# Optimization experiments

Measured on AMD Instinct MI355X. Metric: run time of the kernel, lower is better.

The kernel has to match this reference:

```python
import jax, jax.numpy as jnp
import numpy as np

FG_THRESH = 0.5
BG_HI = 0.5
BG_LO = 0.0
CLS_LAMBDA = 1.0
BBOX2D_LAMBDA = 1.0
BBOX3D_LAMBDA = 1.0

A, FH, FW, STRIDE = 36, 32, 106, 16  # 36*32*106 = 122112 anchors
B, G, NC = 4, 64, 4


def _smooth_l1(x):
    ax = jnp.abs(x)
    return jnp.where(ax < 1.0, 0.5 * ax * ax, ax - 0.5)


def setup_inputs() -> dict:
    rng = np.random.RandomState(0)
    # anchors: [x1,y1,x2,y2, z, w3d, h3d, l3d, ry], centered at origin
    ws = rng.uniform(16, 256, A).astype(np.float32)
    hs = rng.uniform(16, 256, A).astype(np.float32)
    anchors = np.zeros((A, 9), np.float32)
    anchors[:, 0] = -ws / 2; anchors[:, 1] = -hs / 2
    anchors[:, 2] = ws / 2;  anchors[:, 3] = hs / 2
    anchors[:, 4] = rng.uniform(5, 50, A)
    anchors[:, 5:8] = rng.uniform(1, 5, (A, 3))
    anchors[:, 8] = rng.uniform(-np.pi, np.pi, A)
    # rois = anchors tiled over the feature grid (locate_anchors), col 4 = anchor idx
    sx, sy = np.meshgrid(np.arange(FW) * STRIDE, np.arange(FH) * STRIDE)
    shifts = np.stack([sx.ravel(), sy.ravel(), sx.ravel(), sy.ravel()], 1).astype(np.float32)
    N = FH * FW * A
    rois = np.zeros((N, 5), np.float32)
    rois[:, :4] = (shifts[:, None, :] + anchors[None, :, :4]).reshape(-1, 4)
    rois[:, 4] = np.tile(np.arange(A), FH * FW)
    # GT 2D boxes (x1,y1,x2,y2) inside the 1696x512 image
    gcx = rng.uniform(0, FW * STRIDE, (B, G)); gcy = rng.uniform(0, FH * STRIDE, (B, G))
    gw = rng.uniform(30, 200, (B, G)); gh = rng.uniform(30, 200, (B, G))
    gt_boxes = np.stack([gcx - gw / 2, gcy - gh / 2, gcx + gw / 2, gcy + gh / 2], -1).astype(np.float32)
    # GT 3D: projected 3D center (u,v), z, w3d, h3d, l3d, ry
    gt_boxes_3d = np.stack([
        gcx, gcy,
        rng.uniform(5, 50, (B, G)),
        rng.uniform(1, 5, (B, G)), rng.uniform(1, 5, (B, G)), rng.uniform(1, 5, (B, G)),
        rng.uniform(-np.pi, np.pi, (B, G)),
    ], -1).astype(np.float32)
    gt_labels = rng.randint(1, NC, (B, G)).astype(np.int32)
    bbox_means = (rng.randn(1, 11) * 0.01).astype(np.float32)
    bbox_stds = (0.1 + rng.rand(1, 11) * 0.2).astype(np.float32)
    key = jax.random.key(0)
    k1, k2, k3, k4 = jax.random.split(key, 4)
    return {
        "cls": jax.random.normal(k1, (B, N, NC), jnp.float32),
        "prob": jax.random.uniform(k2, (B, N, NC), jnp.float32),
        "bbox_2d": 0.1 * jax.random.normal(k3, (B, N, 4), jnp.float32),
        "bbox_3d": 0.1 * jax.random.normal(k4, (B, N, 7), jnp.float32),
        "rois": jnp.asarray(rois),
        "anchors": jnp.asarray(anchors),
        "bbox_means": jnp.asarray(bbox_means),
        "bbox_stds": jnp.asarray(bbox_stds),
        "gt_boxes": jnp.asarray(gt_boxes),
        "gt_boxes_3d": jnp.asarray(gt_boxes_3d),
        "gt_labels": jnp.asarray(gt_labels),
    }


def _loss(cls, prob, bbox_2d, bbox_3d, rois, anchors, bbox_means, bbox_stds,
          gt_boxes, gt_boxes_3d, gt_labels):
    # anchor geometry (the +1.0 convention matches the torch code)
    widths = rois[:, 2] - rois[:, 0] + 1.0          # [N]
    heights = rois[:, 3] - rois[:, 1] + 1.0
    ctr_x = rois[:, 0] + 0.5 * widths
    ctr_y = rois[:, 1] + 0.5 * heights
    aidx = rois[:, 4].astype(jnp.int32)
    src = anchors[aidx]                             # [N,9] gathered anchors

    # IoU between every roi and every GT: [B,N,G]
    rx1 = rois[None, :, None, 0]; ry1 = rois[None, :, None, 1]
    rx2 = rois[None, :, None, 2]; ry2 = rois[None, :, None, 3]
    gx1 = gt_boxes[:, None, :, 0]; gy1 = gt_boxes[:, None, :, 1]
    gx2 = gt_boxes[:, None, :, 2]; gy2 = gt_boxes[:, None, :, 3]
    iw = jnp.clip(jnp.minimum(rx2, gx2) - jnp.maximum(rx1, gx1) + 1.0, 0.0)
    ih = jnp.clip(jnp.minimum(ry2, gy2) - jnp.maximum(ry1, gy1) + 1.0, 0.0)
    inter = iw * ih
    area_r = (rx2 - rx1 + 1.0) * (ry2 - ry1 + 1.0)
    area_g = (gx2 - gx1 + 1.0) * (gy2 - gy1 + 1.0)
    ols = inter / (area_r + area_g - inter)         # [B,N,G]

    best_iou = jnp.max(ols, axis=-1)                # [B,N]
    best_gt = jnp.argmax(ols, axis=-1)              # [B,N]

    fg = best_iou >= FG_THRESH
    bg = (best_iou < BG_HI) & (best_iou >= BG_LO) & (~fg)

    matched_lbl = jnp.take_along_axis(gt_labels, best_gt, axis=1)   # [B,N]
    labels = jnp.where(fg, matched_lbl, 0)

    gb = jnp.take_along_axis(gt_boxes, best_gt[..., None], axis=1)  # [B,N,4]
    gw = gb[..., 2] - gb[..., 0] + 1.0
    gh = gb[..., 3] - gb[..., 1] + 1.0
    gcx = gb[..., 0] + 0.5 * gw
    gcy = gb[..., 1] + 0.5 * gh
    t2d = jnp.stack([
        (gcx - ctr_x) / widths,
        (gcy - ctr_y) / heights,
        jnp.log(gw / widths),
        jnp.log(gh / heights),
    ], -1)
    t2d = (t2d - bbox_means[0, 0:4]) / bbox_stds[0, 0:4]

    g3 = jnp.take_along_axis(gt_boxes_3d, best_gt[..., None], axis=1)  # [B,N,7]
    t3d = jnp.stack([
        (g3[..., 0] - ctr_x) / widths,
        (g3[..., 1] - ctr_y) / heights,
        g3[..., 2] - src[:, 4],
        jnp.log(g3[..., 3] / src[:, 5]),
        jnp.log(g3[..., 4] / src[:, 6]),
        jnp.log(g3[..., 5] / src[:, 7]),
        g3[..., 6] - src[:, 8],
    ], -1)
    t3d = (t3d - bbox_means[0, 4:11]) / bbox_stds[0, 4:11]

    # ---- losses
    w_fg = fg.astype(cls.dtype)
    n_fg = jnp.maximum(jnp.sum(w_fg), 1.0)
    loss_b2d = jnp.sum(jnp.sum(_smooth_l1(bbox_2d - t2d), -1) * w_fg) / n_fg
    loss_b3d = jnp.sum(jnp.sum(_smooth_l1(bbox_3d - t3d), -1) * w_fg) / n_fg

    w_cls = (fg | bg).astype(cls.dtype)
    logp = jax.nn.log_softmax(cls, axis=-1)
    ce = -jnp.take_along_axis(logp, labels[..., None], axis=-1)[..., 0]
    loss_cls = jnp.sum(ce * w_cls) / jnp.maximum(jnp.sum(w_cls), 1.0)

    return CLS_LAMBDA * loss_cls + BBOX2D_LAMBDA * loss_b2d + BBOX3D_LAMBDA * loss_b3d


def reference(cls, prob, bbox_2d, bbox_3d, rois, anchors, bbox_means, bbox_stds,
              gt_boxes, gt_boxes_3d, gt_labels):
    return _loss(cls, prob, bbox_2d, bbox_3d, rois, anchors, bbox_means, bbox_stds,
                 gt_boxes, gt_boxes_3d, gt_labels)
```

## Files before the change

kernel.cpp:

```cpp
#include <hip/hip_runtime.h>
#include <math.h>

#define AA 36
#define FWW 106
#define NTOT 122112
#define BB 4
#define GG 64
#define STRIDE_PX 16

constexpr int BLOCK = 256;
constexpr int BLOCKS_PER_B = NTOT / BLOCK;
constexpr int NBLK = BB * BLOCKS_PER_B;
#define FBIG 3.402823466e+38f

__device__ __forceinline__ float smooth_l1(float x) {
    float ax = fabsf(x);
    return (ax < 1.0f) ? 0.5f * ax * ax : ax - 0.5f;
}
__device__ __forceinline__ float frcp(float x) { return __builtin_amdgcn_rcpf(x); }

__global__ __launch_bounds__(BLOCK) void rpn_loss_main(
    const float* __restrict__ cls,
    const float* __restrict__ bbox2d,
    const float* __restrict__ bbox3d,
    const float* __restrict__ anchors,
    const float* __restrict__ means,
    const float* __restrict__ stds,
    const float* __restrict__ gt_boxes,
    const float* __restrict__ gt3d,
    const int*   __restrict__ gt_labels,
    float4* __restrict__ part)
{
    __shared__ float4 s_gt4[GG];
    __shared__ float  s_gS[GG];
    __shared__ int    s_gidx[GG];
    __shared__ float  s_anch[AA * 12];
    __shared__ float4 s_red[4];
    __shared__ int    s_K;

    const int tid  = threadIdx.x;
    const int lane = tid & 63;
    const int wv   = tid >> 6;
    const int b    = blockIdx.x / BLOCKS_PER_B;
    const int bpos = blockIdx.x % BLOCKS_PER_B;
    const int n0   = bpos * BLOCK;

    const float4* __restrict__ gtb = reinterpret_cast<const float4*>(gt_boxes) + b * GG;

    if (tid < 64) {
        float mnx = FBIG, mny = FBIG, mxx = -FBIG, mxy = -FBIG;
        if (lane < AA) {
            float a[9];
            #pragma unroll
            for (int k = 0; k < 9; ++k) a[k] = anchors[lane * 9 + k];
            #pragma unroll
            for (int k = 0; k < 9; ++k) s_anch[lane * 12 + k] = a[k];
            const float aw = a[2] - a[0] + 1.0f;
            const float ah = a[3] - a[1] + 1.0f;
            s_anch[lane * 12 + 9]  = aw;
            s_anch[lane * 12 + 10] = ah;
            s_anch[lane * 12 + 11] = 0.0f;
            mnx = a[0]; mny = a[1]; mxx = a[2]; mxy = a[3];
        }
        #pragma unroll
        for (int m = 1; m < 64; m <<= 1) {
            mnx = fminf(mnx, __shfl_xor(mnx, m, 64));
            mny = fminf(mny, __shfl_xor(mny, m, 64));
            mxx = fmaxf(mxx, __shfl_xor(mxx, m, 64));
            mxy = fmaxf(mxy, __shfl_xor(mxy, m, 64));
        }
        const int s0  = n0 / AA;
        const int s1  = (n0 + BLOCK - 1) / AA;
        const int sy0 = s0 / FWW, sy1 = s1 / FWW;
        int sx0 = s0 % FWW, sx1 = s1 % FWW;
        if (sy0 != sy1) { sx0 = 0; sx1 = FWW - 1; }
        const float bx1  = (float)(sx0 * STRIDE_PX) + mnx;
        const float bx2p = (float)(sx1 * STRIDE_PX) + mxx + 1.0f;
        const float by1  = (float)(sy0 * STRIDE_PX) + mny;
        const float by2p = (float)(sy1 * STRIDE_PX) + mxy + 1.0f;

        const float4 gt = gtb[lane];
        const float gz1p = gt.z + 1.0f;
        const float gw1p = gt.w + 1.0f;
        const bool pass = (fminf(bx2p, gz1p) > fmaxf(bx1, gt.x)) &&
                          (fminf(by2p, gw1p) > fmaxf(by1, gt.y));
        const unsigned long long mask = __ballot(pass);
        if (pass) {
            const int pos = __popcll(mask & ((1ull << lane) - 1ull));
            s_gt4[pos]  = make_float4(gt.x, gt.y, gz1p, gw1p);
            s_gS[pos]   = (gz1p - gt.x) * (gw1p - gt.y);
            s_gidx[pos] = lane;
        }
        if (lane == 0) s_K = __popcll(mask);
    }
    __syncthreads();

    const int n     = n0 + tid;
    const int aidx  = n % AA;
    const int shift = n / AA;
    const float sx  = (float)((shift % FWW) * STRIDE_PX);
    const float sy  = (float)((shift / FWW) * STRIDE_PX);
    const float* an = &s_anch[aidx * 12];
    const float aw  = an[9];
    const float ah  = an[10];
    const float x1  = sx + an[0];
    const float y1  = sy + an[1];
    const float x2p = x1 + aw;
    const float y2p = y1 + ah;
    const float ar  = aw * ah;

    const size_t row = (size_t)b * NTOT + n;
    const float4 c = reinterpret_cast<const float4*>(cls)[row];

    const int K = s_K;
    float bi = 0.0f;
    float bS = 1.0f;
    int   bk = 0;
    #pragma unroll 2
    for (int k = 0; k < K; ++k) {
        const float4 g4 = s_gt4[k];
        const float  Sg = s_gS[k];
        const float iw = fminf(x2p, g4.z) - fmaxf(x1, g4.x);
        const float ih = fmaxf(fminf(y2p, g4.w) - fmaxf(y1, g4.y), 0.0f);
        const float inter = iw * ih;
        const float S     = ar + Sg;
        const bool upd = inter * bS > bi * S;
        bi = upd ? inter : bi;
        bS = upd ? S     : bS;
        bk = upd ? k     : bk;
    }
    const bool fg = (3.0f * bi >= bS);

    const float lse = __logf(__expf(c.x) + __expf(c.y) + __expf(c.z) + __expf(c.w));
    int label = 0;
    if (fg) label = gt_labels[b * GG + s_gidx[bk]];
    const float csel = (label == 0) ? c.x : (label == 1) ? c.y :
                       (label == 2) ? c.z : c.w;
    const float ce = lse - csel;

    float l2 = 0.0f, l3 = 0.0f;
    if (fg) {
        const int   bg  = s_gidx[bk];
        const float cx  = x1 + 0.5f * aw;
        const float cy  = y1 + 0.5f * ah;
        const float rw  = frcp(aw);
        const float rh  = frcp(ah);
        const float4 gq = s_gt4[bk];
        const float gw_ = gq.z - gq.x;
        const float gh_ = gq.w - gq.y;
        const float gcx = gq.x + 0.5f * gw_;
        const float gcy = gq.y + 0.5f * gh_;
        float t2[4];
        t2[0] = (gcx - cx) * rw;
        t2[1] = (gcy - cy) * rh;
        t2[2] = __logf(gw_ * rw);
        t2[3] = __logf(gh_ * rh);
        const float4 p2 = reinterpret_cast<const float4*>(bbox2d)[row];
        const float p2a[4] = {p2.x, p2.y, p2.z, p2.w};
        #pragma unroll
        for (int k = 0; k < 4; ++k)
            l2 += smooth_l1(p2a[k] - (t2[k] - means[k]) * frcp(stds[k]));

        const float* g3 = gt3d + ((size_t)b * GG + bg) * 7;
        float t3[7];
        t3[0] = (g3[0] - cx) * rw;
        t3[1] = (g3[1] - cy) * rh;
        t3[2] = g3[2] - an[4];
        t3[3] = __logf(g3[3] * frcp(an[5]));
        t3[4] = __logf(g3[4] * frcp(an[6]));
        t3[5] = __logf(g3[5] * frcp(an[7]));
        t3[6] = g3[6] - an[8];
        const float* p3 = bbox3d + row * 7;
        #pragma unroll
        for (int k = 0; k < 7; ++k)
            l3 += smooth_l1(p3[k] - (t3[k] - means[4 + k]) * frcp(stds[4 + k]));
    }

    float v[4] = {ce, fg ? 1.0f : 0.0f, l2, l3};
    #pragma unroll
    for (int k = 0; k < 4; ++k) {
        float x = v[k];
        #pragma unroll
        for (int off = 32; off > 0; off >>= 1) x += __shfl_down(x, off, 64);
        v[k] = x;
    }
    if (lane == 0) s_red[wv] = make_float4(v[0], v[1], v[2], v[3]);
    __syncthreads();
    if (tid == 0) {
        float4 t;
        t.x = s_red[0].x + s_red[1].x + s_red[2].x + s_red[3].x;
        t.y = s_red[0].y + s_red[1].y + s_red[2].y + s_red[3].y;
        t.z = s_red[0].z + s_red[1].z + s_red[2].z + s_red[3].z;
        t.w = s_red[0].w + s_red[1].w + s_red[2].w + s_red[3].w;
        part[blockIdx.x] = t;
    }
}

__global__ __launch_bounds__(256) void rpn_loss_fin(
    const float4* __restrict__ part, float* __restrict__ out)
{
    __shared__ float4 sh[4];
    float4 s = make_float4(0.f, 0.f, 0.f, 0.f);
    for (int i = threadIdx.x; i < NBLK; i += 256) {
        const float4 p = part[i];
        s.x += p.x; s.y += p.y; s.z += p.z; s.w += p.w;
    }
    #pragma unroll
    for (int off = 32; off > 0; off >>= 1) {
        s.x += __shfl_down(s.x, off, 64);
        s.y += __shfl_down(s.y, off, 64);
        s.z += __shfl_down(s.z, off, 64);
        s.w += __shfl_down(s.w, off, 64);
    }
    const int lane = threadIdx.x & 63;
    const int wv   = threadIdx.x >> 6;
    if (lane == 0) sh[wv] = s;
    __syncthreads();
    if (threadIdx.x == 0) {
        float ce = 0.f, nfg = 0.f, l2 = 0.f, l3 = 0.f;
        #pragma unroll
        for (int i = 0; i < 4; ++i) {
            ce += sh[i].x; nfg += sh[i].y; l2 += sh[i].z; l3 += sh[i].w;
        }
        out[0] = ce / (float)(BB * NTOT) + (l2 + l3) / fmaxf(nfg, 1.0f);
    }
}

extern "C" void kernel_launch(void* const* d_in, const int* in_sizes, int n_in,
                              void* d_out, int out_size, void* d_ws, size_t ws_size,
                              hipStream_t stream) {
    const float* cls     = (const float*)d_in[0];
    const float* bbox2d  = (const float*)d_in[2];
    const float* bbox3d  = (const float*)d_in[3];
    const float* anchors = (const float*)d_in[5];
    const float* means   = (const float*)d_in[6];
    const float* stds    = (const float*)d_in[7];
    const float* gtb     = (const float*)d_in[8];
    const float* gt3     = (const float*)d_in[9];
    const int*   glbl    = (const int*)d_in[10];
    float4* part = (float4*)d_ws;
    float*  out  = (float*)d_out;

    rpn_loss_main<<<dim3(NBLK), BLOCK, 0, stream>>>(cls, bbox2d, bbox3d, anchors,
                                                    means, stds, gtb, gt3, glbl, part);
    rpn_loss_fin<<<1, 256, 0, stream>>>(part, out);
}
```

Before: 18.40 us.

## Cull GT boxes per block by IoU upper bound and reduce via atomics

The per-block GT prefilter now tests each GT against every anchor shape at the block's shift range. It keeps a GT only if an upper bound on IoU could reach the foreground threshold, which should shrink K in the per-anchor IoU loop. The per-block partial sums are now atomically added into 64 accumulator lines, so the finalize kernel is a single wave. A memset launch is added to zero those lines. The cls load is also hoisted before the setup barrier to overlap with it. The risks are a 36-iteration setup loop per block, extra launch overhead from the memset, and correctness that depends on max IoU below threshold always meaning background.

```diff
diff --git a/kernel.cpp b/kernel.cpp
--- a/kernel.cpp
+++ b/kernel.cpp
@@ -11,7 +11,7 @@
 constexpr int BLOCK = 256;
 constexpr int BLOCKS_PER_B = NTOT / BLOCK;
 constexpr int NBLK = BB * BLOCKS_PER_B;
-#define FBIG 3.402823466e+38f
+constexpr int NLINES = 64;
 
 __device__ __forceinline__ float smooth_l1(float x) {
     float ax = fabsf(x);
@@ -29,7 +29,7 @@
     const float* __restrict__ gt_boxes,
     const float* __restrict__ gt3d,
     const int*   __restrict__ gt_labels,
-    float4* __restrict__ part)
+    float* __restrict__ acc)
 {
     __shared__ float4 s_gt4[GG];
     __shared__ float  s_gS[GG];
@@ -47,55 +47,63 @@
 
     const float4* __restrict__ gtb = reinterpret_cast<const float4*>(gt_boxes) + b * GG;
 
+    const int    n   = n0 + tid;
+    const size_t row = (size_t)b * NTOT + n;
+    const float4 c = reinterpret_cast<const float4*>(cls)[row];
+
     if (tid < 64) {
-        float mnx = FBIG, mny = FBIG, mxx = -FBIG, mxy = -FBIG;
         if (lane < AA) {
             float a[9];
             #pragma unroll
             for (int k = 0; k < 9; ++k) a[k] = anchors[lane * 9 + k];
             #pragma unroll
             for (int k = 0; k < 9; ++k) s_anch[lane * 12 + k] = a[k];
-            const float aw = a[2] - a[0] + 1.0f;
-            const float ah = a[3] - a[1] + 1.0f;
-            s_anch[lane * 12 + 9]  = aw;
-            s_anch[lane * 12 + 10] = ah;
+            s_anch[lane * 12 + 9]  = a[2] - a[0] + 1.0f;
+            s_anch[lane * 12 + 10] = a[3] - a[1] + 1.0f;
             s_anch[lane * 12 + 11] = 0.0f;
-            mnx = a[0]; mny = a[1]; mxx = a[2]; mxy = a[3];
-        }
-        #pragma unroll
-        for (int m = 1; m < 64; m <<= 1) {
-            mnx = fminf(mnx, __shfl_xor(mnx, m, 64));
-            mny = fminf(mny, __shfl_xor(mny, m, 64));
-            mxx = fmaxf(mxx, __shfl_xor(mxx, m, 64));
-            mxy = fmaxf(mxy, __shfl_xor(mxy, m, 64));
         }
         const int s0  = n0 / AA;
         const int s1  = (n0 + BLOCK - 1) / AA;
         const int sy0 = s0 / FWW, sy1 = s1 / FWW;
         int sx0 = s0 % FWW, sx1 = s1 % FWW;
         if (sy0 != sy1) { sx0 = 0; sx1 = FWW - 1; }
-        const float bx1  = (float)(sx0 * STRIDE_PX) + mnx;
-        const float bx2p = (float)(sx1 * STRIDE_PX) + mxx + 1.0f;
-        const float by1  = (float)(sy0 * STRIDE_PX) + mny;
-        const float by2p = (float)(sy1 * STRIDE_PX) + mxy + 1.0f;
+        const float fx0 = (float)(sx0 * STRIDE_PX);
+        const float fx1 = (float)(sx1 * STRIDE_PX);
+        const float fy0 = (float)(sy0 * STRIDE_PX);
+        const float fy1 = (float)(sy1 * STRIDE_PX);
 
         const float4 gt = gtb[lane];
         const float gz1p = gt.z + 1.0f;
         const float gw1p = gt.w + 1.0f;
-        const bool pass = (fminf(bx2p, gz1p) > fmaxf(bx1, gt.x)) &&
-                          (fminf(by2p, gw1p) > fmaxf(by1, gt.y));
+        const float gw_  = gz1p - gt.x;
+        const float gh_  = gw1p - gt.y;
+        const float ag   = gw_ * gh_;
+
+        bool pass = false;
+        for (int a = 0; a < AA; ++a) {
+            const float ax1  = s_anch[a * 12 + 0];
+            const float ay1  = s_anch[a * 12 + 1];
+            const float ax2p = s_anch[a * 12 + 2] + 1.0f;
+            const float ay2p = s_anch[a * 12 + 3] + 1.0f;
+            const float aw   = s_anch[a * 12 + 9];
+            const float ah   = s_anch[a * 12 + 10];
+            float iwub = fminf(fx1 + ax2p, gz1p) - fmaxf(fx0 + ax1, gt.x);
+            float ihub = fminf(fy1 + ay2p, gw1p) - fmaxf(fy0 + ay1, gt.y);
+            iwub = fmaxf(fminf(iwub, aw), 0.0f);
+            ihub = fmaxf(fminf(ihub, ah), 0.0f);
+            pass |= (3.0f * iwub * ihub >= aw * ah + ag);
+        }
         const unsigned long long mask = __ballot(pass);
         if (pass) {
             const int pos = __popcll(mask & ((1ull << lane) - 1ull));
             s_gt4[pos]  = make_float4(gt.x, gt.y, gz1p, gw1p);
-            s_gS[pos]   = (gz1p - gt.x) * (gw1p - gt.y);
+            s_gS[pos]   = ag;
             s_gidx[pos] = lane;
         }
         if (lane == 0) s_K = __popcll(mask);
     }
     __syncthreads();
 
-    const int n     = n0 + tid;
     const int aidx  = n % AA;
     const int shift = n / AA;
     const float sx  = (float)((shift % FWW) * STRIDE_PX);
@@ -108,9 +116,6 @@
     const float x2p = x1 + aw;
     const float y2p = y1 + ah;
     const float ar  = aw * ah;
-
-    const size_t row = (size_t)b * NTOT + n;
-    const float4 c = reinterpret_cast<const float4*>(cls)[row];
 
     const int K = s_K;
     float bi = 0.0f;
@@ -187,43 +192,27 @@
     if (lane == 0) s_red[wv] = make_float4(v[0], v[1], v[2], v[3]);
     __syncthreads();
     if (tid == 0) {
-        float4 t;
-        t.x = s_red[0].x + s_red[1].x + s_red[2].x + s_red[3].x;
-        t.y = s_red[0].y + s_red[1].y + s_red[2].y + s_red[3].y;
-        t.z = s_red[0].z + s_red[1].z + s_red[2].z + s_red[3].z;
-        t.w = s_red[0].w + s_red[1].w + s_red[2].w + s_red[3].w;
-        part[blockIdx.x] = t;
-    }
-}
-
-__global__ __launch_bounds__(256) void rpn_loss_fin(
-    const float4* __restrict__ part, float* __restrict__ out)
+        float* line = acc + (blockIdx.x & (NLINES - 1)) * 4;
+        atomicAdd(line + 0, s_red[0].x + s_red[1].x + s_red[2].x + s_red[3].x);
+        atomicAdd(line + 1, s_red[0].y + s_red[1].y + s_red[2].y + s_red[3].y);
+        atomicAdd(line + 2, s_red[0].z + s_red[1].z + s_red[2].z + s_red[3].z);
+        atomicAdd(line + 3, s_red[0].w + s_red[1].w + s_red[2].w + s_red[3].w);
+    }
+}
+
+__global__ __launch_bounds__(64) void rpn_loss_fin(
+    const float4* __restrict__ acc, float* __restrict__ out)
 {
-    __shared__ float4 sh[4];
-    float4 s = make_float4(0.f, 0.f, 0.f, 0.f);
-    for (int i = threadIdx.x; i < NBLK; i += 256) {
-        const float4 p = part[i];
-        s.x += p.x; s.y += p.y; s.z += p.z; s.w += p.w;
-    }
+    float4 p = acc[threadIdx.x];
     #pragma unroll
-    for (int off = 32; off > 0; off >>= 1) {
-        s.x += __shfl_down(s.x, off, 64);
-        s.y += __shfl_down(s.y, off, 64);
-        s.z += __shfl_down(s.z, off, 64);
-        s.w += __shfl_down(s.w, off, 64);
-    }
-    const int lane = threadIdx.x & 63;
-    const int wv   = threadIdx.x >> 6;
-    if (lane == 0) sh[wv] = s;
-    __syncthreads();
-    if (threadIdx.x == 0) {
-        float ce = 0.f, nfg = 0.f, l2 = 0.f, l3 = 0.f;
-        #pragma unroll
-        for (int i = 0; i < 4; ++i) {
-            ce += sh[i].x; nfg += sh[i].y; l2 += sh[i].z; l3 += sh[i].w;
-        }
-        out[0] = ce / (float)(BB * NTOT) + (l2 + l3) / fmaxf(nfg, 1.0f);
-    }
+    for (int m = 1; m < 64; m <<= 1) {
+        p.x += __shfl_xor(p.x, m, 64);
+        p.y += __shfl_xor(p.y, m, 64);
+        p.z += __shfl_xor(p.z, m, 64);
+        p.w += __shfl_xor(p.w, m, 64);
+    }
+    if (threadIdx.x == 0)
+        out[0] = p.x / (float)(BB * NTOT) + (p.z + p.w) / fmaxf(p.y, 1.0f);
 }
 
 extern "C" void kernel_launch(void* const* d_in, const int* in_sizes, int n_in,
@@ -238,10 +227,11 @@
     const float* gtb     = (const float*)d_in[8];
     const float* gt3     = (const float*)d_in[9];
     const int*   glbl    = (const int*)d_in[10];
-    float4* part = (float4*)d_ws;
-    float*  out  = (float*)d_out;
-
+    float* acc = (float*)d_ws;
+    float* out = (float*)d_out;
+
+    hipMemsetAsync(acc, 0, NLINES * 4 * sizeof(float), stream);
     rpn_loss_main<<<dim3(NBLK), BLOCK, 0, stream>>>(cls, bbox2d, bbox3d, anchors,
-                                                    means, stds, gtb, gt3, glbl, part);
-    rpn_loss_fin<<<1, 256, 0, stream>>>(part, out);
-}
+                                                    means, stds, gtb, gt3, glbl, acc);
+    rpn_loss_fin<<<1, 64, 0, stream>>>((const float4*)acc, out);
+}
```

Measured after the change: 28.20 us. 53.2% more time.

## Cull GT boxes per block with an IoU upper bound and hoist loads before barrier

Applied to the files above, without the earlier changes.

The per-block GT culling now loops over all 36 anchors. For each anchor it computes an upper bound on the intersection and keeps a GT only if that bound could still reach the foreground IoU threshold. This should shrink the per-thread argmax loop over candidate GTs well below the earlier plain bounding-box overlap test. The classification load, anchor geometry and log-sum-exp are also moved ahead of the shared-memory setup and barrier so their latency overlaps with it. In exchange, the first wave does a 36-iteration serial loop before the barrier, which delays every thread in the block.

```diff
diff --git a/kernel.cpp b/kernel.cpp
--- a/kernel.cpp
+++ b/kernel.cpp
@@ -11,7 +11,6 @@
 constexpr int BLOCK = 256;
 constexpr int BLOCKS_PER_B = NTOT / BLOCK;
 constexpr int NBLK = BB * BLOCKS_PER_B;
-#define FBIG 3.402823466e+38f
 
 __device__ __forceinline__ float smooth_l1(float x) {
     float ax = fabsf(x);
@@ -47,70 +46,78 @@
 
     const float4* __restrict__ gtb = reinterpret_cast<const float4*>(gt_boxes) + b * GG;
 
+    const int    n   = n0 + tid;
+    const size_t row = (size_t)b * NTOT + n;
+    const float4 c = reinterpret_cast<const float4*>(cls)[row];
+
+    const int aidx  = n % AA;
+    const int shift = n / AA;
+    const float sx  = (float)((shift % FWW) * STRIDE_PX);
+    const float sy  = (float)((shift / FWW) * STRIDE_PX);
+    const float a0 = anchors[aidx * 9 + 0];
+    const float a1 = anchors[aidx * 9 + 1];
+    const float a2 = anchors[aidx * 9 + 2];
+    const float a3 = anchors[aidx * 9 + 3];
+    const float aw  = a2 - a0 + 1.0f;
+    const float ah  = a3 - a1 + 1.0f;
+    const float x1  = sx + a0;
+    const float y1  = sy + a1;
+    const float x2p = x1 + aw;
+    const float y2p = y1 + ah;
+    const float ar  = aw * ah;
+
+    const float lse = __logf(__expf(c.x) + __expf(c.y) + __expf(c.z) + __expf(c.w));
+
     if (tid < 64) {
-        float mnx = FBIG, mny = FBIG, mxx = -FBIG, mxy = -FBIG;
         if (lane < AA) {
             float a[9];
             #pragma unroll
             for (int k = 0; k < 9; ++k) a[k] = anchors[lane * 9 + k];
             #pragma unroll
             for (int k = 0; k < 9; ++k) s_anch[lane * 12 + k] = a[k];
-            const float aw = a[2] - a[0] + 1.0f;
-            const float ah = a[3] - a[1] + 1.0f;
-            s_anch[lane * 12 + 9]  = aw;
-            s_anch[lane * 12 + 10] = ah;
+            s_anch[lane * 12 + 9]  = a[2] - a[0] + 1.0f;
+            s_anch[lane * 12 + 10] = a[3] - a[1] + 1.0f;
             s_anch[lane * 12 + 11] = 0.0f;
-            mnx = a[0]; mny = a[1]; mxx = a[2]; mxy = a[3];
-        }
-        #pragma unroll
-        for (int m = 1; m < 64; m <<= 1) {
-            mnx = fminf(mnx, __shfl_xor(mnx, m, 64));
-            mny = fminf(mny, __shfl_xor(mny, m, 64));
-            mxx = fmaxf(mxx, __shfl_xor(mxx, m, 64));
-            mxy = fmaxf(mxy, __shfl_xor(mxy, m, 64));
         }
         const int s0  = n0 / AA;
         const int s1  = (n0 + BLOCK - 1) / AA;
         const int sy0 = s0 / FWW, sy1 = s1 / FWW;
         int sx0 = s0 % FWW, sx1 = s1 % FWW;
         if (sy0 != sy1) { sx0 = 0; sx1 = FWW - 1; }
-        const float bx1  = (float)(sx0 * STRIDE_PX) + mnx;
-        const float bx2p = (float)(sx1 * STRIDE_PX) + mxx + 1.0f;
-        const float by1  = (float)(sy0 * STRIDE_PX) + mny;
-        const float by2p = (float)(sy1 * STRIDE_PX) + mxy + 1.0f;
+        const float fx0 = (float)(sx0 * STRIDE_PX);
+        const float fx1 = (float)(sx1 * STRIDE_PX);
+        const float fy0 = (float)(sy0 * STRIDE_PX);
+        const float fy1 = (float)(sy1 * STRIDE_PX);
 
         const float4 gt = gtb[lane];
         const float gz1p = gt.z + 1.0f;
         const float gw1p = gt.w + 1.0f;
-        const bool pass = (fminf(bx2p, gz1p) > fmaxf(bx1, gt.x)) &&
-                          (fminf(by2p, gw1p) > fmaxf(by1, gt.y));
+        const float ag   = (gz1p - gt.x) * (gw1p - gt.y);
+
+        bool pass = false;
+        for (int a = 0; a < AA; ++a) {
+            const float ax1  = s_anch[a * 12 + 0];
+            const float ay1  = s_anch[a * 12 + 1];
+            const float ax2p = s_anch[a * 12 + 2] + 1.0f;
+            const float ay2p = s_anch[a * 12 + 3] + 1.0f;
+            const float aaw  = s_anch[a * 12 + 9];
+            const float aah  = s_anch[a * 12 + 10];
+            float iwub = fminf(fx1 + ax2p, gz1p) - fmaxf(fx0 + ax1, gt.x);
+            float ihub = fminf(fy1 + ay2p, gw1p) - fmaxf(fy0 + ay1, gt.y);
+            iwub = fmaxf(fminf(iwub, aaw), 0.0f);
+            ihub = fmaxf(fminf(ihub, aah), 0.0f);
+            pass |= (3.0f * iwub * ihub >= aaw * aah + ag);
+        }
         const unsigned long long mask = __ballot(pass);
         if (pass) {
             const int pos = __popcll(mask & ((1ull << lane) - 1ull));
             s_gt4[pos]  = make_float4(gt.x, gt.y, gz1p, gw1p);
-            s_gS[pos]   = (gz1p - gt.x) * (gw1p - gt.y);
+            s_gS[pos]   = ag;
             s_gidx[pos] = lane;
         }
         if (lane == 0) s_K = __popcll(mask);
     }
     __syncthreads();
-
-    const int n     = n0 + tid;
-    const int aidx  = n % AA;
-    const int shift = n / AA;
-    const float sx  = (float)((shift % FWW) * STRIDE_PX);
-    const float sy  = (float)((shift / FWW) * STRIDE_PX);
-    const float* an = &s_anch[aidx * 12];
-    const float aw  = an[9];
-    const float ah  = an[10];
-    const float x1  = sx + an[0];
-    const float y1  = sy + an[1];
-    const float x2p = x1 + aw;
-    const float y2p = y1 + ah;
-    const float ar  = aw * ah;
-
-    const size_t row = (size_t)b * NTOT + n;
-    const float4 c = reinterpret_cast<const float4*>(cls)[row];
 
     const int K = s_K;
     float bi = 0.0f;
@@ -131,7 +138,6 @@
     }
     const bool fg = (3.0f * bi >= bS);
 
-    const float lse = __logf(__expf(c.x) + __expf(c.y) + __expf(c.z) + __expf(c.w));
     int label = 0;
     if (fg) label = gt_labels[b * GG + s_gidx[bk]];
     const float csel = (label == 0) ? c.x : (label == 1) ? c.y :
@@ -161,6 +167,7 @@
         for (int k = 0; k < 4; ++k)
             l2 += smooth_l1(p2a[k] - (t2[k] - means[k]) * frcp(stds[k]));
 
+        const float* an = &s_anch[aidx * 12];
         const float* g3 = gt3d + ((size_t)b * GG + bg) * 7;
         float t3[7];
         t3[0] = (g3[0] - cx) * rw;
```

Result: no change. 18.22 us (-1.0%).

## Tighten per-block GT culling with anchor-aware IoU bound and enlarge blocks

Applied to the files above, without the earlier changes.

Block size doubles to 512 with tail guarding. The per-block GT prefilter now tests, for each anchor and the extreme shift positions in the block, whether IoU could reach the foreground threshold, instead of a loose bounding-box overlap. This shrinks the GT candidate list K for the inner IoU loop. The cls load is hoisted before the prefilter, anchors are packed into float4 in shared memory, and the reduction is trimmed to three values, with the fg count taken by ballot. The costs are extra prefilter work across all waves plus an added sync, and the culling bound must be correct or foreground assignment changes.

```diff
diff --git a/kernel.cpp b/kernel.cpp
--- a/kernel.cpp
+++ b/kernel.cpp
@@ -8,10 +8,10 @@
 #define GG 64
 #define STRIDE_PX 16
 
-constexpr int BLOCK = 256;
-constexpr int BLOCKS_PER_B = NTOT / BLOCK;
+constexpr int BLOCK = 512;
+constexpr int NW    = BLOCK / 64;
+constexpr int BLOCKS_PER_B = (NTOT + BLOCK - 1) / BLOCK;
 constexpr int NBLK = BB * BLOCKS_PER_B;
-#define FBIG 3.402823466e+38f
 
 __device__ __forceinline__ float smooth_l1(float x) {
     float ax = fabsf(x);
@@ -34,111 +34,136 @@
     __shared__ float4 s_gt4[GG];
     __shared__ float  s_gS[GG];
     __shared__ int    s_gidx[GG];
-    __shared__ float  s_anch[AA * 12];
-    __shared__ float4 s_red[4];
+    __shared__ float4 s_anch4[AA];
+    __shared__ float  s_anch[AA * 13];
+    __shared__ unsigned long long s_bal[NW];
+    __shared__ float4 s_red[16];
     __shared__ int    s_K;
 
     const int tid  = threadIdx.x;
     const int lane = tid & 63;
     const int wv   = tid >> 6;
+    const int wvu  = __builtin_amdgcn_readfirstlane(wv);
     const int b    = blockIdx.x / BLOCKS_PER_B;
     const int bpos = blockIdx.x % BLOCKS_PER_B;
     const int n0   = bpos * BLOCK;
+    const int n    = n0 + tid;
+    const bool valid = (n < NTOT);
 
     const float4* __restrict__ gtb = reinterpret_cast<const float4*>(gt_boxes) + b * GG;
 
-    if (tid < 64) {
-        float mnx = FBIG, mny = FBIG, mxx = -FBIG, mxy = -FBIG;
-        if (lane < AA) {
-            float a[9];
-            #pragma unroll
-            for (int k = 0; k < 9; ++k) a[k] = anchors[lane * 9 + k];
-            #pragma unroll
-            for (int k = 0; k < 9; ++k) s_anch[lane * 12 + k] = a[k];
-            const float aw = a[2] - a[0] + 1.0f;
-            const float ah = a[3] - a[1] + 1.0f;
-            s_anch[lane * 12 + 9]  = aw;
-            s_anch[lane * 12 + 10] = ah;
-            s_anch[lane * 12 + 11] = 0.0f;
-            mnx = a[0]; mny = a[1]; mxx = a[2]; mxy = a[3];
-        }
-        #pragma unroll
-        for (int m = 1; m < 64; m <<= 1) {
-            mnx = fminf(mnx, __shfl_xor(mnx, m, 64));
-            mny = fminf(mny, __shfl_xor(mny, m, 64));
-            mxx = fmaxf(mxx, __shfl_xor(mxx, m, 64));
-            mxy = fmaxf(mxy, __shfl_xor(mxy, m, 64));
-        }
-        const int s0  = n0 / AA;
-        const int s1  = (n0 + BLOCK - 1) / AA;
-        const int sy0 = s0 / FWW, sy1 = s1 / FWW;
-        int sx0 = s0 % FWW, sx1 = s1 % FWW;
-        if (sy0 != sy1) { sx0 = 0; sx1 = FWW - 1; }
-        const float bx1  = (float)(sx0 * STRIDE_PX) + mnx;
-        const float bx2p = (float)(sx1 * STRIDE_PX) + mxx + 1.0f;
-        const float by1  = (float)(sy0 * STRIDE_PX) + mny;
-        const float by2p = (float)(sy1 * STRIDE_PX) + mxy + 1.0f;
-
-        const float4 gt = gtb[lane];
-        const float gz1p = gt.z + 1.0f;
-        const float gw1p = gt.w + 1.0f;
-        const bool pass = (fminf(bx2p, gz1p) > fmaxf(bx1, gt.x)) &&
-                          (fminf(by2p, gw1p) > fmaxf(by1, gt.y));
-        const unsigned long long mask = __ballot(pass);
-        if (pass) {
+    const size_t row = (size_t)b * NTOT + n;
+    float4 c = make_float4(0.f, 0.f, 0.f, 0.f);
+    if (valid) c = reinterpret_cast<const float4*>(cls)[row];
+
+    if (tid < AA) {
+        float a[9];
+        #pragma unroll
+        for (int k = 0; k < 9; ++k) a[k] = anchors[tid * 9 + k];
+        #pragma unroll
+        for (int k = 0; k < 9; ++k) s_anch[tid * 13 + k] = a[k];
+        s_anch4[tid] = make_float4(a[0], a[1], a[2] - a[0] + 1.0f, a[3] - a[1] + 1.0f);
+    }
+
+    const int nlast = (n0 + BLOCK - 1 < NTOT) ? (n0 + BLOCK - 1) : (NTOT - 1);
+    const int s0  = n0 / AA,  s1  = nlast / AA;
+    const int sy0 = s0 / FWW, sy1 = s1 / FWW;
+    float fxA0, fxA1, fyA, fxB0, fxB1, fyB;
+    if (sy0 == sy1) {
+        fxA0 = (float)((s0 % FWW) * STRIDE_PX); fxA1 = (float)((s1 % FWW) * STRIDE_PX);
+        fyA  = (float)(sy0 * STRIDE_PX);
+        fxB0 = fxA0; fxB1 = fxA1; fyB = fyA;
+    } else {
+        fxA0 = (float)((s0 % FWW) * STRIDE_PX); fxA1 = (float)((FWW - 1) * STRIDE_PX);
+        fyA  = (float)(sy0 * STRIDE_PX);
+        fxB0 = 0.0f;                            fxB1 = (float)((s1 % FWW) * STRIDE_PX);
+        fyB  = (float)(sy1 * STRIDE_PX);
+    }
+
+    const float4 gt   = gtb[lane];
+    const float  gz1p = gt.z + 1.0f;
+    const float  gw1p = gt.w + 1.0f;
+    const float  ag   = (gz1p - gt.x) * (gw1p - gt.y);
+
+    bool pass = false;
+    for (int a = wvu; a < AA; a += NW) {
+        const float ax1 = anchors[a * 9 + 0];
+        const float ay1 = anchors[a * 9 + 1];
+        const float aw  = anchors[a * 9 + 2] - ax1 + 1.0f;
+        const float ah  = anchors[a * 9 + 3] - ay1 + 1.0f;
+        const float thr = aw * ah + ag;
+        float iwA = fminf(fxA1 + ax1 + aw, gz1p) - fmaxf(fxA0 + ax1, gt.x);
+        float ihA = fminf(fyA  + ay1 + ah, gw1p) - fmaxf(fyA  + ay1, gt.y);
+        iwA = fmaxf(fminf(iwA, aw), 0.0f);
+        ihA = fmaxf(fminf(ihA, ah), 0.0f);
+        pass |= (3.0f * iwA * ihA >= thr);
+        float iwB = fminf(fxB1 + ax1 + aw, gz1p) - fmaxf(fxB0 + ax1, gt.x);
+        float ihB = fminf(fyB  + ay1 + ah, gw1p) - fmaxf(fyB  + ay1, gt.y);
+        iwB = fmaxf(fminf(iwB, aw), 0.0f);
+        ihB = fmaxf(fminf(ihB, ah), 0.0f);
+        pass |= (3.0f * iwB * ihB >= thr);
+    }
+    const unsigned long long wmask = __ballot(pass);
+    if (lane == 0) s_bal[wv] = wmask;
+    __syncthreads();
+
+    if (wv == 0) {
+        unsigned long long mask = 0ull;
+        #pragma unroll
+        for (int j = 0; j < NW; ++j) mask |= s_bal[j];
+        if ((mask >> lane) & 1ull) {
             const int pos = __popcll(mask & ((1ull << lane) - 1ull));
             s_gt4[pos]  = make_float4(gt.x, gt.y, gz1p, gw1p);
-            s_gS[pos]   = (gz1p - gt.x) * (gw1p - gt.y);
+            s_gS[pos]   = ag;
             s_gidx[pos] = lane;
         }
         if (lane == 0) s_K = __popcll(mask);
-    }
-    __syncthreads();
-
-    const int n     = n0 + tid;
+        if (lane >= NW && lane < 16) s_red[lane] = make_float4(0.f, 0.f, 0.f, 0.f);
+    }
+    __syncthreads();
+
     const int aidx  = n % AA;
     const int shift = n / AA;
     const float sx  = (float)((shift % FWW) * STRIDE_PX);
     const float sy  = (float)((shift / FWW) * STRIDE_PX);
-    const float* an = &s_anch[aidx * 12];
-    const float aw  = an[9];
-    const float ah  = an[10];
-    const float x1  = sx + an[0];
-    const float y1  = sy + an[1];
+    const float4 A4 = s_anch4[aidx];
+    const float aw  = A4.z;
+    const float ah  = A4.w;
+    const float x1  = sx + A4.x;
+    const float y1  = sy + A4.y;
     const float x2p = x1 + aw;
     const float y2p = y1 + ah;
     const float ar  = aw * ah;
 
-    const size_t row = (size_t)b * NTOT + n;
-    const float4 c = reinterpret_cast<const float4*>(cls)[row];
+    const float lse = __logf(__expf(c.x) + __expf(c.y) + __expf(c.z) + __expf(c.w));
 
     const int K = s_K;
-    float bi = 0.0f;
-    float bS = 1.0f;
+    float bi = 0.0f, bS = 1.0f;
     int   bk = 0;
-    #pragma unroll 2
-    for (int k = 0; k < K; ++k) {
-        const float4 g4 = s_gt4[k];
-        const float  Sg = s_gS[k];
-        const float iw = fminf(x2p, g4.z) - fmaxf(x1, g4.x);
-        const float ih = fmaxf(fminf(y2p, g4.w) - fmaxf(y1, g4.y), 0.0f);
-        const float inter = iw * ih;
-        const float S     = ar + Sg;
-        const bool upd = inter * bS > bi * S;
-        bi = upd ? inter : bi;
-        bS = upd ? S     : bS;
-        bk = upd ? k     : bk;
-    }
-    const bool fg = (3.0f * bi >= bS);
-
-    const float lse = __logf(__expf(c.x) + __expf(c.y) + __expf(c.z) + __expf(c.w));
+    if (valid) {
+        #pragma unroll 2
+        for (int k = 0; k < K; ++k) {
+            const float4 g4 = s_gt4[k];
+            const float  Sg = s_gS[k];
+            const float iw = fminf(x2p, g4.z) - fmaxf(x1, g4.x);
+            const float ih = fmaxf(fminf(y2p, g4.w) - fmaxf(y1, g4.y), 0.0f);
+            const float inter = iw * ih;
+            const float S     = ar + Sg;
+            const bool upd = inter * bS > bi * S;
+            bi = upd ? inter : bi;
+            bS = upd ? S     : bS;
+            bk = upd ? k     : bk;
+        }
+    }
+    const bool fg = valid && (3.0f * bi >= bS);
+
     int label = 0;
     if (fg) label = gt_labels[b * GG + s_gidx[bk]];
     const float csel = (label == 0) ? c.x : (label == 1) ? c.y :
                        (label == 2) ? c.z : c.w;
-    const float ce = lse - csel;
-
-    float l2 = 0.0f, l3 = 0.0f;
+    const float ce = valid ? (lse - csel) : 0.0f;
+
+    float l23 = 0.0f;
     if (fg) {
         const int   bg  = s_gidx[bk];
         const float cx  = x1 + 0.5f * aw;
@@ -159,8 +184,9 @@
         const float p2a[4] = {p2.x, p2.y, p2.z, p2.w};
         #pragma unroll
         for (int k = 0; k < 4; ++k)
-            l2 += smooth_l1(p2a[k] - (t2[k] - means[k]) * frcp(stds[k]));
-
+            l23 += smooth_l1(p2a[k] - (t2[k] - means[k]) * frcp(stds[k]));
+
+        const float* an = &s_anch[aidx * 13];
         const float* g3 = gt3d + ((size_t)b * GG + bg) * 7;
         float t3[7];
         t3[0] = (g3[0] - cx) * rw;
@@ -173,26 +199,27 @@
         const float* p3 = bbox3d + row * 7;
         #pragma unroll
         for (int k = 0; k < 7; ++k)
-            l3 += smooth_l1(p3[k] - (t3[k] - means[4 + k]) * frcp(stds[4 + k]));
-    }
-
-    float v[4] = {ce, fg ? 1.0f : 0.0f, l2, l3};
+            l23 += smooth_l1(p3[k] - (t3[k] - means[4 + k]) * frcp(stds[4 + k]));
+    }
+
+    float vce = ce, vl = l23;
     #pragma unroll
-    for (int k = 0; k < 4; ++k) {
-        float x = v[k];
-        #pragma unroll
-        for (int off = 32; off > 0; off >>= 1) x += __shfl_down(x, off, 64);
-        v[k] = x;
-    }
-    if (lane == 0) s_red[wv] = make_float4(v[0], v[1], v[2], v[3]);
-    __syncthreads();
-    if (tid == 0) {
-        float4 t;
-        t.x = s_red[0].x + s_red[1].x + s_red[2].x + s_red[3].x;
-        t.y = s_red[0].y + s_red[1].y + s_red[2].y + s_red[3].y;
-        t.z = s_red[0].z + s_red[1].z + s_red[2].z + s_red[3].z;
-        t.w = s_red[0].w + s_red[1].w + s_red[2].w + s_red[3].w;
-        part[blockIdx.x] = t;
+    for (int off = 32; off > 0; off >>= 1) {
+        vce += __shfl_down(vce, off, 64);
+        vl  += __shfl_down(vl,  off, 64);
+    }
+    const float nfgw = (float)__popcll(__ballot(fg));
+    if (lane == 0) s_red[wv] = make_float4(vce, vl, nfgw, 0.f);
+    __syncthreads();
+    if (tid < 16) {
+        float4 p = s_red[tid];
+        #pragma unroll
+        for (int m = 1; m < 16; m <<= 1) {
+            p.x += __shfl_xor(p.x, m, 64);
+            p.y += __shfl_xor(p.y, m, 64);
+            p.z += __shfl_xor(p.z, m, 64);
+        }
+        if (tid == 0) part[blockIdx.x] = p;
     }
 }
 
@@ -203,26 +230,25 @@
     float4 s = make_float4(0.f, 0.f, 0.f, 0.f);
     for (int i = threadIdx.x; i < NBLK; i += 256) {
         const float4 p = part[i];
-        s.x += p.x; s.y += p.y; s.z += p.z; s.w += p.w;
+        s.x += p.x; s.y += p.y; s.z += p.z;
     }
     #pragma unroll
     for (int off = 32; off > 0; off >>= 1) {
         s.x += __shfl_down(s.x, off, 64);
         s.y += __shfl_down(s.y, off, 64);
         s.z += __shfl_down(s.z, off, 64);
-        s.w += __shfl_down(s.w, off, 64);
     }
     const int lane = threadIdx.x & 63;
     const int wv   = threadIdx.x >> 6;
     if (lane == 0) sh[wv] = s;
     __syncthreads();
     if (threadIdx.x == 0) {
-        float ce = 0.f, nfg = 0.f, l2 = 0.f, l3 = 0.f;
+        float ce = 0.f, l23 = 0.f, nfg = 0.f;
         #pragma unroll
         for (int i = 0; i < 4; ++i) {
-            ce += sh[i].x; nfg += sh[i].y; l2 += sh[i].z; l3 += sh[i].w;
-        }
-        out[0] = ce / (float)(BB * NTOT) + (l2 + l3) / fmaxf(nfg, 1.0f);
+            ce += sh[i].x; l23 += sh[i].y; nfg += sh[i].z;
+        }
+        out[0] = ce / (float)((size_t)BB * NTOT) + l23 / fmaxf(nfg, 1.0f);
     }
 }
 
```

Result: faster. 15.98 us (-13.2%).
